# Kernel tuning notes

Measured on AMD Instinct MI355X. Metric: run time of the kernel, lower is better.

The kernel has to match this reference:

```python
import math
import jax, jax.numpy as jnp
import numpy as np

B, T, H, DH, DV = 4, 4096, 16, 128, 128
CHUNK = 1024
ROPE_BASE = 10000.0
NEG = -1e30


def setup_inputs() -> dict:
    key = jax.random.key(0)
    kq, kk, kv = jax.random.split(key, 3)
    q = jax.random.normal(kq, (B, T, H, DH), dtype=jnp.float32)
    k = jax.random.normal(kk, (B, T, H, DH), dtype=jnp.float32)
    v = jax.random.normal(kv, (B, T, H, DV), dtype=jnp.float32)
    return {"q": q, "k": k, "v": v, "start_index": 0}


def _rope_tables(start, length, dh):
    half = dh // 2
    inv_freq = jnp.exp(jnp.arange(half, dtype=jnp.float32) * -(math.log(ROPE_BASE) / half))
    pos = start + jnp.arange(length, dtype=jnp.float32)
    ang = pos[:, None] * inv_freq[None, :]  # (T, half)
    # broadcast over batch and heads: (1, T, 1, half)
    return jnp.cos(ang)[None, :, None, :], jnp.sin(ang)[None, :, None, :]


def _rotate(x, cos, sin):
    x1, x2 = jnp.split(x, 2, axis=-1)
    return jnp.concatenate([x1 * cos - x2 * sin, x2 * cos + x1 * sin], axis=-1)


def reference(q, k, v, start_index):
    b, t, h, dh = q.shape
    dv = v.shape[-1]
    cos, sin = _rope_tables(start_index, t, dh)
    q_rot = _rotate(q, cos, sin)
    k_rot = _rotate(k, cos, sin)

    nc = t // CHUNK
    qc = q_rot.reshape(b, nc, CHUNK, h, dh)
    kc = k_rot.reshape(b, nc, CHUNK, h, dh)
    vc = v.reshape(b, nc, CHUNK, h, dv)

    # Normalized attention: no 1/sqrt(d) temperature (scale = 1.0)
    scores = jnp.einsum("bnqhd,bnkhd->bnhqk", qc, kc)
    causal = jnp.tril(jnp.ones((CHUNK, CHUNK), dtype=bool))
    scores = jnp.where(causal, scores, NEG)
    attn = jax.nn.softmax(scores, axis=-1)
    out = jnp.einsum("bnhqk,bnkhd->bnqhd", attn, vc)
    return out.reshape(b, t, h, dv)
```

## Files before the change

### kernel.cpp

```cpp
#include <hip/hip_runtime.h>
#include <math.h>

#define Tsz 4096
#define Hn 16
#define DHc 128
#define DVc 128
#define CHK 1024
#define NEGV (-1e30f)
#define ROPE_C 0.14391156831f

typedef float f32x4 __attribute__((ext_vector_type(4)));
typedef short s16x8 __attribute__((ext_vector_type(8)));
typedef unsigned short u16t;
typedef u16t u16x8 __attribute__((ext_vector_type(8)));
typedef u16t u16x4 __attribute__((ext_vector_type(4)));

__device__ __forceinline__ u16t f2bf(float x){
  union { float f; unsigned u; } cv; cv.f = x;
  unsigned r = cv.u + 0x7fffu + ((cv.u >> 16) & 1u);
  return (u16t)(r >> 16);
}
__device__ __forceinline__ float bf2f(u16t h){
  union { float f; unsigned u; } cv; cv.u = ((unsigned)h) << 16;
  return cv.f;
}
__device__ __forceinline__ f32x4 mfma16(u16x8 a, u16x8 b, f32x4 c){
  return __builtin_amdgcn_mfma_f32_16x16x32_bf16(
      __builtin_bit_cast(s16x8, a), __builtin_bit_cast(s16x8, b), c, 0, 0, 0);
}

__global__ void rope_table_kernel(const int* __restrict__ start,
                                  float* __restrict__ tab){
  const int idx = blockIdx.x * 256 + threadIdx.x;
  const int t = idx >> 6, d = idx & 63;
  const float inv = expf(-(float)d * ROPE_C);
  const float ang = (float)(start[0] + t) * inv;
  float s, c;
  sincosf(ang, &s, &c);
  tab[idx] = c;
  tab[Tsz * 64 + idx] = s;
}

template<int MODE>
__global__ __launch_bounds__(1024, 4)
void mega_attn_kernel(const float* __restrict__ q, const float* __restrict__ k,
                      const float* __restrict__ v, const float* __restrict__ tab,
                      const int* __restrict__ start, float* __restrict__ out)
{
  __shared__ __align__(16) u16t sKhi[64 * 128];
  __shared__ __align__(16) u16t sKlo[64 * 128];
  __shared__ __align__(16) u16t sVhi[128 * 64];
  __shared__ __align__(16) u16t sVlo[128 * 64];
  __shared__ __align__(16) u16t sP[16][1024];

  const int bid  = blockIdx.x;
  const int xcd  = bid & 7;
  const int jj   = bid >> 3;
  const int prob = xcd * 32 + (jj & 31);
  const int qt   = jj >> 5;
  const int b  = prob >> 6;
  const int ch = (prob >> 4) & 3;
  const int h  = prob & 15;

  const int tid  = threadIdx.x;
  const int w    = tid >> 6;
  const int lane = tid & 63;
  const int g    = lane >> 4;
  const int lc   = lane & 15;

  const float* cosT = tab;
  const float* sinT = tab + (size_t)Tsz * 64;
  const int tab0 = ch * CHK;
  int st = 0;
  if constexpr (MODE == 1) st = start[0];

  const size_t bh = ((size_t)b * Tsz + (size_t)ch * CHK) * Hn + h;
  const float* qbase = q + bh * DHc;
  const float* kbase = k + bh * DHc;
  const float* vbase = v + bh * DVc;
  float* obase = out + bh * DVc;
  const int rs = Hn * DHc;

  const int qrow0 = 256 * qt + 16 * w;
  u16t* myP = &sP[w][0];

  u16t* qscratch = (w < 4 ? sKhi : w < 8 ? sKlo : w < 12 ? sVhi : sVlo)
                   + (size_t)(w & 3) * 2048;

  u16x8 qhi[4], qlo[4];
  {
    const int srow = lane >> 2;
    const int c4   = lane & 3;
    const int swz  = (srow & 7) << 3;
    const int rck = qrow0 + srow;
    const float* qp = qbase + (size_t)rck * rs + 16 * c4;
    f32x4 A[4], Bv[4], Cv[4], Sv[4];
    #pragma unroll
    for (int m = 0; m < 4; ++m){
      A[m]  = *(const f32x4*)(qp + 4 * m);
      Bv[m] = *(const f32x4*)(qp + 64 + 4 * m);
    }
    if constexpr (MODE == 0){
      const float* cp = cosT + (size_t)(tab0 + rck) * 64 + 16 * c4;
      const float* sp = sinT + (size_t)(tab0 + rck) * 64 + 16 * c4;
      #pragma unroll
      for (int m = 0; m < 4; ++m){
        Cv[m] = *(const f32x4*)(cp + 4 * m);
        Sv[m] = *(const f32x4*)(sp + 4 * m);
      }
    } else {
      const float pbase = (float)(st + tab0 + rck);
      #pragma unroll
      for (int m = 0; m < 16; ++m){
        const float inv = expf(-(float)(16 * c4 + m) * ROPE_C);
        float ss, cc;
        sincosf(pbase * inv, &ss, &cc);
        Cv[m >> 2][m & 3] = cc;
        Sv[m >> 2][m & 3] = ss;
      }
    }
    float r1[16], r2[16];
    u16t h1[16], h2[16];
    #pragma unroll
    for (int m = 0; m < 16; ++m){
      const float xa = A[m >> 2][m & 3];
      const float xb = Bv[m >> 2][m & 3];
      const float co = Cv[m >> 2][m & 3];
      const float si = Sv[m >> 2][m & 3];
      r1[m] = xa * co - xb * si;
      r2[m] = xb * co + xa * si;
      h1[m] = f2bf(r1[m]);
      h2[m] = f2bf(r2[m]);
    }
    u16x8 w0, w1, w2, w3;
    #pragma unroll
    for (int m = 0; m < 8; ++m){
      w0[m] = h1[m]; w1[m] = h1[m + 8];
      w2[m] = h2[m]; w3[m] = h2[m + 8];
    }
    *(u16x8*)(qscratch + ((srow * 128 + 16 * c4     ) ^ swz)) = w0;
    *(u16x8*)(qscratch + ((srow * 128 + 16 * c4 + 8 ) ^ swz)) = w1;
    *(u16x8*)(qscratch + ((srow * 128 + 16 * c4 + 64) ^ swz)) = w2;
    *(u16x8*)(qscratch + ((srow * 128 + 16 * c4 + 72) ^ swz)) = w3;
    #pragma unroll
    for (int ks = 0; ks < 4; ++ks)
      qhi[ks] = *(const u16x8*)(qscratch + ((lc * 128 + ks * 32 + g * 8) ^ ((lc & 7) << 3)));
    #pragma unroll
    for (int m = 0; m < 8; ++m){
      w0[m] = f2bf(r1[m]     - bf2f(h1[m]));
      w1[m] = f2bf(r1[m + 8] - bf2f(h1[m + 8]));
      w2[m] = f2bf(r2[m]     - bf2f(h2[m]));
      w3[m] = f2bf(r2[m + 8] - bf2f(h2[m + 8]));
    }
    *(u16x8*)(qscratch + ((srow * 128 + 16 * c4     ) ^ swz)) = w0;
    *(u16x8*)(qscratch + ((srow * 128 + 16 * c4 + 8 ) ^ swz)) = w1;
    *(u16x8*)(qscratch + ((srow * 128 + 16 * c4 + 64) ^ swz)) = w2;
    *(u16x8*)(qscratch + ((srow * 128 + 16 * c4 + 72) ^ swz)) = w3;
    #pragma unroll
    for (int ks = 0; ks < 4; ++ks)
      qlo[ks] = *(const u16x8*)(qscratch + ((lc * 128 + ks * 32 + g * 8) ^ ((lc & 7) << 3)));
  }
  __syncthreads();

  const f32x4 vzero = {0.f, 0.f, 0.f, 0.f};
  f32x4 acc[8];
  #pragma unroll
  for (int dt = 0; dt < 8; ++dt) acc[dt] = vzero;
  float mrow[4], lrow[4];
  #pragma unroll
  for (int i = 0; i < 4; ++i){ mrow[i] = -INFINITY; lrow[i] = 0.f; }

  const int ntiles = 4 * (qt + 1);
  const int krow = tid >> 4;
  const int ka   = tid & 15;

  for (int t = 0; t < ntiles; ++t){
    {
      const int kr = t * 64 + krow;
      const float* kp = kbase + (size_t)kr * rs;
      f32x4 xa = *(const f32x4*)(kp + 4 * ka);
      f32x4 xb = *(const f32x4*)(kp + 4 * ka + 64);
      f32x4 cc, ss;
      if constexpr (MODE == 0){
        cc = *(const f32x4*)(cosT + (size_t)(tab0 + kr) * 64 + 4 * ka);
        ss = *(const f32x4*)(sinT + (size_t)(tab0 + kr) * 64 + 4 * ka);
      } else {
        const float pbase = (float)(st + tab0 + kr);
        #pragma unroll
        for (int m = 0; m < 4; ++m){
          const float inv = expf(-(float)(4 * ka + m) * ROPE_C);
          float s1, c1;
          sincosf(pbase * inv, &s1, &c1);
          cc[m] = c1; ss[m] = s1;
        }
      }
      u16x4 hh1, ll1, hh2, ll2;
      #pragma unroll
      for (int m = 0; m < 4; ++m){
        const float r1 = xa[m] * cc[m] - xb[m] * ss[m];
        const float r2 = xb[m] * cc[m] + xa[m] * ss[m];
        const u16t a1h = f2bf(r1); hh1[m] = a1h; ll1[m] = f2bf(r1 - bf2f(a1h));
        const u16t a2h = f2bf(r2); hh2[m] = a2h; ll2[m] = f2bf(r2 - bf2f(a2h));
      }
      const int e1 = (krow * 128 + 4 * ka) ^ ((krow & 7) << 3);
      *(u16x4*)(sKhi + e1)      = hh1; *(u16x4*)(sKlo + e1)      = ll1;
      *(u16x4*)(sKhi + e1 + 64) = hh2; *(u16x4*)(sKlo + e1 + 64) = ll2;

      const float* vp = vbase + (size_t)kr * rs + 8 * ka;
      f32x4 v0 = *(const f32x4*)(vp);
      f32x4 v1 = *(const f32x4*)(vp + 4);
      #pragma unroll
      for (int m = 0; m < 8; ++m){
        const int dv = 8 * ka + m;
        const float xv = (m < 4) ? v0[m & 3] : v1[m & 3];
        const u16t vh = f2bf(xv);
        const int ve = (dv * 64 + krow) ^ ((((dv & 7) ^ ((dv >> 3) & 7))) << 3);
        sVhi[ve] = vh;
        sVlo[ve] = f2bf(xv - bf2f(vh));
      }
    }
    __syncthreads();

    const int kmin = t * 64;
    if (kmin <= qrow0 + 15){
      f32x4 S[4];
      #pragma unroll
      for (int ct = 0; ct < 4; ++ct){
        f32x4 s0v = vzero;
        const int krw = 16 * ct + lc;
        const int swk = (krw & 7) << 3;
        #pragma unroll
        for (int ks = 0; ks < 4; ++ks){
          const int ke = (krw * 128 + 32 * ks + 8 * g) ^ swk;
          const u16x8 bh = *(const u16x8*)(sKhi + ke);
          const u16x8 bl = *(const u16x8*)(sKlo + ke);
          s0v = mfma16(qhi[ks], bh, s0v);
          s0v = mfma16(qlo[ks], bh, s0v);
          s0v = mfma16(qhi[ks], bl, s0v);
        }
        S[ct] = s0v;
      }
      if (kmin + 63 > qrow0){
        #pragma unroll
        for (int ct = 0; ct < 4; ++ct){
          const int key = kmin + 16 * ct + lc;
          #pragma unroll
          for (int i = 0; i < 4; ++i){
            if (key > qrow0 + 4 * g + i) S[ct][i] = NEGV;
          }
        }
      }
      #pragma unroll
      for (int i = 0; i < 4; ++i){
        float tm = fmaxf(fmaxf(S[0][i], S[1][i]), fmaxf(S[2][i], S[3][i]));
        tm = fmaxf(tm, __shfl_xor(tm, 1));
        tm = fmaxf(tm, __shfl_xor(tm, 2));
        tm = fmaxf(tm, __shfl_xor(tm, 4));
        tm = fmaxf(tm, __shfl_xor(tm, 8));
        const float mnew = fmaxf(mrow[i], tm);
        const float sc = __expf(mrow[i] - mnew);
        float ps = 0.f;
        u16t pb[4];
        #pragma unroll
        for (int ct = 0; ct < 4; ++ct){
          const float p = __expf(S[ct][i] - mnew);
          ps += p;
          pb[ct] = f2bf(p);
        }
        ps += __shfl_xor(ps, 1);
        ps += __shfl_xor(ps, 2);
        ps += __shfl_xor(ps, 4);
        ps += __shfl_xor(ps, 8);
        lrow[i] = lrow[i] * sc + ps;
        mrow[i] = mnew;
        #pragma unroll
        for (int dt = 0; dt < 8; ++dt) acc[dt][i] *= sc;
        const int prow = 4 * g + i;
        const int swp = (prow & 7) << 3;
        #pragma unroll
        for (int ct = 0; ct < 4; ++ct)
          myP[(prow * 64 + 16 * ct + lc) ^ swp] = pb[ct];
      }
      #pragma unroll
      for (int kvs = 0; kvs < 2; ++kvs){
        const u16x8 pa = *(const u16x8*)(myP + ((lc * 64 + kvs * 32 + 8 * g) ^ ((lc & 7) << 3)));
        #pragma unroll
        for (int dt = 0; dt < 8; ++dt){
          const int dv = 16 * dt + lc;
          const int ve = (dv * 64 + kvs * 32 + 8 * g) ^ (((dv & 7) ^ ((dv >> 3) & 7)) << 3);
          const u16x8 vh = *(const u16x8*)(sVhi + ve);
          const u16x8 vl = *(const u16x8*)(sVlo + ve);
          acc[dt] = mfma16(pa, vh, acc[dt]);
          acc[dt] = mfma16(pa, vl, acc[dt]);
        }
      }
    }
    __syncthreads();
  }

  #pragma unroll
  for (int i = 0; i < 4; ++i){
    const float rl = 1.f / lrow[i];
    const int rck = qrow0 + 4 * g + i;
    float* op = obase + (size_t)rck * rs + lc;
    #pragma unroll
    for (int dt = 0; dt < 8; ++dt)
      op[16 * dt] = acc[dt][i] * rl;
  }
}

extern "C" void kernel_launch(void* const* d_in, const int* in_sizes, int n_in,
                              void* d_out, int out_size, void* d_ws, size_t ws_size,
                              hipStream_t stream) {
  const float* q = (const float*)d_in[0];
  const float* k = (const float*)d_in[1];
  const float* v = (const float*)d_in[2];
  const int* start = (const int*)d_in[3];
  float* out = (float*)d_out;
  float* tab = (float*)d_ws;

  const size_t need = (size_t)2 * Tsz * 64 * sizeof(float);
  if (ws_size >= need){
    rope_table_kernel<<<dim3((Tsz * 64) / 256), dim3(256), 0, stream>>>(start, tab);
    mega_attn_kernel<0><<<dim3(1024), dim3(1024), 0, stream>>>(q, k, v, tab, start, out);
  } else {
    mega_attn_kernel<1><<<dim3(1024), dim3(1024), 0, stream>>>(q, k, v, tab, start, out);
  }
}
```

Before: 1.483 ms.

## Prefetch next K/V tile into registers and remap block-to-problem ordering

Global loads of the next K/V tile, plus the RoPE cos/sin values, are now issued into registers right after the barrier. Their latency can then hide behind the current tile's MFMA work instead of stalling at the top of each iteration. The block index mapping also changes so the four causal query tiles of one problem are consecutive within an XCD, which changes L2 locality and the order in which the uneven-cost tiles are scheduled. The prefetch costs about 24 extra live VGPRs per thread at 1024 threads per block, which may pressure the register budget.

```diff
diff --git a/kernel.cpp b/kernel.cpp
--- a/kernel.cpp
+++ b/kernel.cpp
@@ -55,9 +55,9 @@
 
   const int bid  = blockIdx.x;
   const int xcd  = bid & 7;
-  const int jj   = bid >> 3;
-  const int prob = xcd * 32 + (jj & 31);
-  const int qt   = jj >> 5;
+  const int idx8 = bid >> 3;
+  const int qt   = idx8 & 3;
+  const int prob = xcd * 32 + (idx8 >> 2);
   const int b  = prob >> 6;
   const int ch = (prob >> 4) & 3;
   const int h  = prob & 15;
@@ -174,31 +174,39 @@
   const int krow = tid >> 4;
   const int ka   = tid & 15;
 
+  f32x4 pxa, pxb, pcc, pss, pv0, pv1;
+  auto loadr = [&](int t){
+    const int kr = t * 64 + krow;
+    const float* kp = kbase + (size_t)kr * rs;
+    pxa = *(const f32x4*)(kp + 4 * ka);
+    pxb = *(const f32x4*)(kp + 4 * ka + 64);
+    if constexpr (MODE == 0){
+      pcc = *(const f32x4*)(cosT + (size_t)(tab0 + kr) * 64 + 4 * ka);
+      pss = *(const f32x4*)(sinT + (size_t)(tab0 + kr) * 64 + 4 * ka);
+    } else {
+      const float pbase = (float)(st + tab0 + kr);
+      #pragma unroll
+      for (int m = 0; m < 4; ++m){
+        const float inv = expf(-(float)(4 * ka + m) * ROPE_C);
+        float s1, c1;
+        sincosf(pbase * inv, &s1, &c1);
+        pcc[m] = c1; pss[m] = s1;
+      }
+    }
+    const float* vp = vbase + (size_t)kr * rs + 8 * ka;
+    pv0 = *(const f32x4*)(vp);
+    pv1 = *(const f32x4*)(vp + 4);
+  };
+
+  loadr(0);
+
   for (int t = 0; t < ntiles; ++t){
     {
-      const int kr = t * 64 + krow;
-      const float* kp = kbase + (size_t)kr * rs;
-      f32x4 xa = *(const f32x4*)(kp + 4 * ka);
-      f32x4 xb = *(const f32x4*)(kp + 4 * ka + 64);
-      f32x4 cc, ss;
-      if constexpr (MODE == 0){
-        cc = *(const f32x4*)(cosT + (size_t)(tab0 + kr) * 64 + 4 * ka);
-        ss = *(const f32x4*)(sinT + (size_t)(tab0 + kr) * 64 + 4 * ka);
-      } else {
-        const float pbase = (float)(st + tab0 + kr);
-        #pragma unroll
-        for (int m = 0; m < 4; ++m){
-          const float inv = expf(-(float)(4 * ka + m) * ROPE_C);
-          float s1, c1;
-          sincosf(pbase * inv, &s1, &c1);
-          cc[m] = c1; ss[m] = s1;
-        }
-      }
       u16x4 hh1, ll1, hh2, ll2;
       #pragma unroll
       for (int m = 0; m < 4; ++m){
-        const float r1 = xa[m] * cc[m] - xb[m] * ss[m];
-        const float r2 = xb[m] * cc[m] + xa[m] * ss[m];
+        const float r1 = pxa[m] * pcc[m] - pxb[m] * pss[m];
+        const float r2 = pxb[m] * pcc[m] + pxa[m] * pss[m];
         const u16t a1h = f2bf(r1); hh1[m] = a1h; ll1[m] = f2bf(r1 - bf2f(a1h));
         const u16t a2h = f2bf(r2); hh2[m] = a2h; ll2[m] = f2bf(r2 - bf2f(a2h));
       }
@@ -206,13 +214,10 @@
       *(u16x4*)(sKhi + e1)      = hh1; *(u16x4*)(sKlo + e1)      = ll1;
       *(u16x4*)(sKhi + e1 + 64) = hh2; *(u16x4*)(sKlo + e1 + 64) = ll2;
 
-      const float* vp = vbase + (size_t)kr * rs + 8 * ka;
-      f32x4 v0 = *(const f32x4*)(vp);
-      f32x4 v1 = *(const f32x4*)(vp + 4);
       #pragma unroll
       for (int m = 0; m < 8; ++m){
         const int dv = 8 * ka + m;
-        const float xv = (m < 4) ? v0[m & 3] : v1[m & 3];
+        const float xv = (m < 4) ? pv0[m & 3] : pv1[m & 3];
         const u16t vh = f2bf(xv);
         const int ve = (dv * 64 + krow) ^ ((((dv & 7) ^ ((dv >> 3) & 7))) << 3);
         sVhi[ve] = vh;
@@ -220,6 +225,8 @@
       }
     }
     __syncthreads();
+
+    if (t + 1 < ntiles) loadr(t + 1);
 
     const int kmin = t * 64;
     if (kmin <= qrow0 + 15){
```

Result: slower. 2.106 ms (+42.1%).
